# Kernel tuning notes

Measured on AMD Instinct MI355X. Metric: run time of the kernel, lower is better.

## Reference

```python
import jax, jax.numpy as jnp
import numpy as np
import math

N_EMBD = 1024
N_HEADS = 16
B, T = 4, 2048

def setup_inputs() -> dict:
    key = jax.random.key(0)
    k1, k2, k3 = jax.random.split(key, 3)
    x = jax.random.normal(k1, (B, T, N_EMBD), dtype=jnp.float32)
    scale = 1.0 / math.sqrt(N_EMBD)
    W_attn = jax.random.normal(k2, (N_EMBD, 3 * N_EMBD), dtype=jnp.float32) * scale
    W_proj = jax.random.normal(k3, (N_EMBD, N_EMBD), dtype=jnp.float32) * scale
    return {"x": x, "W_attn": W_attn, "W_proj": W_proj}

def reference(x, W_attn, W_proj):
    Bb, Tt, C = x.shape
    hd = C // N_HEADS
    qkv = x @ W_attn  # [B,T,3C]
    q, k, v = jnp.split(qkv, 3, axis=-1)
    # [B,H,T,hd]
    q = q.reshape(Bb, Tt, N_HEADS, hd).transpose(0, 2, 1, 3)
    k = k.reshape(Bb, Tt, N_HEADS, hd).transpose(0, 2, 1, 3)
    v = v.reshape(Bb, Tt, N_HEADS, hd).transpose(0, 2, 1, 3)
    att = jnp.einsum('bhqd,bhkd->bhqk', q, k) * (1.0 / math.sqrt(hd))
    mask = jnp.tril(jnp.ones((Tt, Tt), dtype=bool))
    att = jnp.where(mask[None, None], att, -jnp.inf)
    att = jax.nn.softmax(att, axis=-1)
    out = jnp.einsum('bhqk,bhkd->bhqd', att, v)
    out = out.transpose(0, 2, 1, 3).reshape(Bb, Tt, C)
    return out @ W_proj
```

## Files before the change

### kernel.cpp

```cpp
#include <hip/hip_runtime.h>
#include <cstddef>
#include <cstdint>

typedef __attribute__((ext_vector_type(8))) _Float16 half8;
typedef __attribute__((ext_vector_type(4))) _Float16 half4;
typedef __attribute__((ext_vector_type(4))) float f32x4;
typedef __attribute__((ext_vector_type(16))) float f32x16;

#define N_EMBD 1024
#define N_HEADS 16
#define BATCH 4
#define SEQ 2048
#define C3 3072
#define HD 64

__device__ inline uint32_t pk2(float x, float y) {
    auto h2 = __builtin_amdgcn_cvt_pkrtz(x, y);
    uint32_t u;
    __builtin_memcpy(&u, &h2, 4);
    return u;
}

__device__ inline void swap32(uint32_t& a, uint32_t& b) {
    asm volatile("v_permlane32_swap_b32 %0, %1" : "+v"(a), "+v"(b));
}

__global__ void cvt_f32_f16(const float* __restrict__ in, _Float16* __restrict__ out, int n) {
    int i = (blockIdx.x * 256 + threadIdx.x) * 4;
    if (i >= n) return;
    float4 v = *(const float4*)(in + i);
    half4 h;
    h[0] = (_Float16)v.x; h[1] = (_Float16)v.y; h[2] = (_Float16)v.z; h[3] = (_Float16)v.w;
    *(half4*)(out + i) = h;
}

__global__ void transpose_cvt(const float* __restrict__ in, _Float16* __restrict__ out,
                              int R, int Ncols) {
    __shared__ float tile[32][33];
    int n0 = blockIdx.x * 32, r0 = blockIdx.y * 32;
    int tx = threadIdx.x, ty = threadIdx.y;
#pragma unroll
    for (int i = 0; i < 32; i += 8)
        tile[ty + i][tx] = in[(size_t)(r0 + ty + i) * Ncols + n0 + tx];
    __syncthreads();
#pragma unroll
    for (int i = 0; i < 32; i += 8)
        out[(size_t)(n0 + ty + i) * R + r0 + tx] = (_Float16)tile[tx][ty + i];
}

__global__ void transpose_v(const _Float16* __restrict__ qkv, _Float16* __restrict__ vT) {
    __shared__ _Float16 tile[32][36];
    int t0 = blockIdx.x * 32;
    int bhd = blockIdx.y;
    int bh = bhd >> 1, dh = bhd & 1;
    int b = bh >> 4, h = bh & 15;
    int tx = threadIdx.x, ty = threadIdx.y;
#pragma unroll
    for (int i = 0; i < 32; i += 8)
        tile[ty + i][tx] = qkv[(size_t)(b * SEQ + t0 + ty + i) * C3 + 2 * N_EMBD + h * HD + dh * 32 + tx];
    __syncthreads();
#pragma unroll
    for (int i = 0; i < 32; i += 8)
        vT[((size_t)bh * HD + dh * 32 + ty + i) * SEQ + t0 + tx] = tile[tx][ty + i];
}

__device__ inline void store1(float* p, float v) { *p = v; }
__device__ inline void store1(_Float16* p, float v) { *p = (_Float16)v; }

template <typename OutT>
__global__ __launch_bounds__(512, 1) void gemm256(
    const _Float16* __restrict__ A, const _Float16* __restrict__ Bt,
    OutT* __restrict__ C, int M, int N, int K) {
    __shared__ _Float16 Al[2][256 * 64];
    __shared__ _Float16 Bl[2][256 * 64];
    const int tid = threadIdx.x;
    const int lane = tid & 63, wave = tid >> 6;
    const int l15 = lane & 15, l4 = lane >> 4;
    const int wm = wave >> 2, wn = wave & 3;

    const int nwg = gridDim.x, nbx = N >> 8;
    int wg = blockIdx.x;
    if ((nwg & 7) == 0) { int cpx = nwg >> 3; wg = (wg & 7) * cpx + (wg >> 3); }
    const int row0 = (wg / nbx) * 256, col0 = (wg % nbx) * 256;
    const int TAU = K >> 6;

    auto stageA = [&](int h, int ts) {
        _Float16* dst = &Al[ts & 1][h * 128 * 64];
#pragma unroll
        for (int i = 0; i < 2; ++i) {
            int idx = tid + 512 * i;
            int usrc = (idx & 7) ^ ((idx >> 3) & 7);
            __builtin_amdgcn_global_load_lds(
                (const __attribute__((address_space(1))) void*)(A + (size_t)(row0 + h * 128 + (idx >> 3)) * K + ts * 64 + usrc * 8),
                (__attribute__((address_space(3))) void*)(dst + idx * 8), 16, 0, 0);
        }
    };
    auto stageB = [&](int h, int ts) {
        _Float16* dst = &Bl[ts & 1][h * 128 * 64];
#pragma unroll
        for (int i = 0; i < 2; ++i) {
            int idx = tid + 512 * i;
            int usrc = (idx & 7) ^ ((idx >> 3) & 7);
            __builtin_amdgcn_global_load_lds(
                (const __attribute__((address_space(1))) void*)(Bt + (size_t)(col0 + h * 128 + (idx >> 3)) * K + ts * 64 + usrc * 8),
                (__attribute__((address_space(3))) void*)(dst + idx * 8), 16, 0, 0);
        }
    };

    f32x4 acc[8][4] = {};
    stageA(0, 0); stageA(1, 0); stageB(0, 0); stageB(1, 0);
    stageA(0, 1); stageA(1, 1); stageB(0, 1); stageB(1, 1);
    asm volatile("s_waitcnt vmcnt(8)" ::: "memory");
    __builtin_amdgcn_s_barrier();

    half8 a[4][2], b0[2][2], b1[2][2];
    for (int tau = 0; tau < TAU; ++tau) {
        const int buf = tau & 1;
        const _Float16* Ab = &Al[buf][0];
        const _Float16* Bb = &Bl[buf][0];
        const int t2ok = (tau + 2 < TAU);

#pragma unroll
        for (int m = 0; m < 4; ++m)
#pragma unroll
            for (int ks = 0; ks < 2; ++ks) {
                int r = wm * 128 + m * 16 + l15;
                a[m][ks] = *(const half8*)(Ab + r * 64 + (((ks * 4 + l4) ^ (r & 7)) * 8));
            }
#pragma unroll
        for (int n = 0; n < 2; ++n)
#pragma unroll
            for (int ks = 0; ks < 2; ++ks) {
                int r = wn * 64 + n * 16 + l15;
                b0[n][ks] = *(const half8*)(Bb + r * 64 + (((ks * 4 + l4) ^ (r & 7)) * 8));
            }
        if (tau + 1 >= 2 && tau + 1 < TAU) stageA(1, tau + 1);
        __builtin_amdgcn_s_barrier();
        __builtin_amdgcn_s_setprio(1);
#pragma unroll
        for (int m = 0; m < 4; ++m)
#pragma unroll
            for (int n = 0; n < 2; ++n)
#pragma unroll
                for (int ks = 0; ks < 2; ++ks)
                    acc[m][n] = __builtin_amdgcn_mfma_f32_16x16x32_f16(a[m][ks], b0[n][ks], acc[m][n], 0, 0, 0);
        __builtin_amdgcn_s_setprio(0);
        __builtin_amdgcn_s_barrier();

#pragma unroll
        for (int n = 0; n < 2; ++n)
#pragma unroll
            for (int ks = 0; ks < 2; ++ks) {
                int r = wn * 64 + 32 + n * 16 + l15;
                b1[n][ks] = *(const half8*)(Bb + r * 64 + (((ks * 4 + l4) ^ (r & 7)) * 8));
            }
        if (t2ok) stageB(0, tau + 2);
        __builtin_amdgcn_s_barrier();
        __builtin_amdgcn_s_setprio(1);
#pragma unroll
        for (int m = 0; m < 4; ++m)
#pragma unroll
            for (int n = 0; n < 2; ++n)
#pragma unroll
                for (int ks = 0; ks < 2; ++ks)
                    acc[m][2 + n] = __builtin_amdgcn_mfma_f32_16x16x32_f16(a[m][ks], b1[n][ks], acc[m][2 + n], 0, 0, 0);
        __builtin_amdgcn_s_setprio(0);
        __builtin_amdgcn_s_barrier();

#pragma unroll
        for (int m = 0; m < 4; ++m)
#pragma unroll
            for (int ks = 0; ks < 2; ++ks) {
                int r = wm * 128 + 64 + m * 16 + l15;
                a[m][ks] = *(const half8*)(Ab + r * 64 + (((ks * 4 + l4) ^ (r & 7)) * 8));
            }
        if (t2ok) stageB(1, tau + 2);
        __builtin_amdgcn_s_barrier();
        __builtin_amdgcn_s_setprio(1);
#pragma unroll
        for (int m = 0; m < 4; ++m)
#pragma unroll
            for (int n = 0; n < 2; ++n)
#pragma unroll
                for (int ks = 0; ks < 2; ++ks)
                    acc[4 + m][2 + n] = __builtin_amdgcn_mfma_f32_16x16x32_f16(a[m][ks], b1[n][ks], acc[4 + m][2 + n], 0, 0, 0);
        __builtin_amdgcn_s_setprio(0);
        __builtin_amdgcn_s_barrier();

        if (t2ok) stageA(0, tau + 2);
        __builtin_amdgcn_s_barrier();
        __builtin_amdgcn_s_setprio(1);
#pragma unroll
        for (int m = 0; m < 4; ++m)
#pragma unroll
            for (int n = 0; n < 2; ++n)
#pragma unroll
                for (int ks = 0; ks < 2; ++ks)
                    acc[4 + m][n] = __builtin_amdgcn_mfma_f32_16x16x32_f16(a[m][ks], b0[n][ks], acc[4 + m][n], 0, 0, 0);
        __builtin_amdgcn_s_setprio(0);
        if (tau <= TAU - 3) {
            asm volatile("s_waitcnt vmcnt(6)" ::: "memory");
        } else if (tau == TAU - 2) {
            asm volatile("s_waitcnt vmcnt(0)" ::: "memory");
        }
        __builtin_amdgcn_s_barrier();
    }

#pragma unroll
    for (int mi = 0; mi < 8; ++mi)
#pragma unroll
        for (int ni = 0; ni < 4; ++ni)
#pragma unroll
            for (int j = 0; j < 4; ++j) {
                int r = row0 + wm * 128 + (mi >> 2) * 64 + (mi & 3) * 16 + l4 * 4 + j;
                int c = col0 + wn * 64 + (ni >> 1) * 32 + (ni & 1) * 16 + l15;
                store1(C + (size_t)r * N + c, acc[mi][ni][j]);
            }
}

template <typename OutT>
__global__ __launch_bounds__(256, 2) void gemm_h(
    const _Float16* __restrict__ A, const _Float16* __restrict__ Bt,
    OutT* __restrict__ C, int M, int N, int K) {
    __shared__ _Float16 Al[128 * 32];
    __shared__ _Float16 Bl[128 * 32];
    const int tid = threadIdx.x;
    const int wave = tid >> 6, lane = tid & 63;
    const int l15 = lane & 15, l4 = lane >> 4;
    const int gx = gridDim.x;
    int lin = blockIdx.y * gx + blockIdx.x;
    int bcol, brow;
    if ((gx & 7) == 0) {
        int cpx = gx >> 3;
        int xcd = lin & 7;
        int idx = lin >> 3;
        bcol = xcd * cpx + idx % cpx;
        brow = idx / cpx;
    } else { bcol = blockIdx.x; brow = blockIdx.y; }
    const int row0 = brow * 128, col0 = bcol * 128;
    const int wm = wave >> 1, wn = wave & 1;
    f32x4 acc[4][4] = {};
    for (int k0 = 0; k0 < K; k0 += 32) {
#pragma unroll
        for (int i = 0; i < 2; ++i) {
            int c = tid + 256 * i;
            int r = c >> 2, c8 = (c & 3) * 8;
            __builtin_amdgcn_global_load_lds(
                (const __attribute__((address_space(1))) void*)(A + (size_t)(row0 + r) * K + k0 + c8),
                (__attribute__((address_space(3))) void*)(Al + (size_t)(wave * 64 + 256 * i) * 8),
                16, 0, 0);
        }
#pragma unroll
        for (int i = 0; i < 2; ++i) {
            int c = tid + 256 * i;
            int r = c >> 2, c8 = (c & 3) * 8;
            __builtin_amdgcn_global_load_lds(
                (const __attribute__((address_space(1))) void*)(Bt + (size_t)(col0 + r) * K + k0 + c8),
                (__attribute__((address_space(3))) void*)(Bl + (size_t)(wave * 64 + 256 * i) * 8),
                16, 0, 0);
        }
        __syncthreads();
        half8 a[4], b[4];
#pragma unroll
        for (int m = 0; m < 4; ++m)
            a[m] = *(const half8*)(Al + (wm * 64 + m * 16 + l15) * 32 + l4 * 8);
#pragma unroll
        for (int n = 0; n < 4; ++n)
            b[n] = *(const half8*)(Bl + (wn * 64 + n * 16 + l15) * 32 + l4 * 8);
        __builtin_amdgcn_s_setprio(1);
#pragma unroll
        for (int m = 0; m < 4; ++m)
#pragma unroll
            for (int n = 0; n < 4; ++n)
                acc[m][n] = __builtin_amdgcn_mfma_f32_16x16x32_f16(a[m], b[n], acc[m][n], 0, 0, 0);
        __builtin_amdgcn_s_setprio(0);
        __syncthreads();
    }
#pragma unroll
    for (int m = 0; m < 4; ++m)
#pragma unroll
        for (int n = 0; n < 4; ++n)
#pragma unroll
            for (int j = 0; j < 4; ++j) {
                int r = row0 + wm * 64 + m * 16 + l4 * 4 + j;
                int cc = col0 + wn * 64 + n * 16 + l15;
                store1(C + (size_t)r * N + cc, acc[m][n][j]);
            }
}

__global__ __launch_bounds__(256, 3) void attn_kernel(const _Float16* __restrict__ qkv,
                                                      const _Float16* __restrict__ vT,
                                                      _Float16* __restrict__ ao) {
    const int bid = blockIdx.x;
    const int qt = 15 - (bid >> 6);
    const int bh = bid & 63;
    const int b = bh >> 4, h = bh & 15;
    const int tid = threadIdx.x, lane = tid & 63;
    const int wave = tid >> 6;
    const int l31 = lane & 31, L = lane >> 5;

    __shared__ _Float16 Kl[3][64 * 64];
    __shared__ _Float16 Vl[3][64 * 64];

    const float qscale = 0.125f * 1.44269504089f;
    const float NEGC = -4.0f * 1.44269504089f;

    const int q0w = qt * 128 + wave * 32;
    const int q_g = q0w + l31;
    const int nt = 2 * qt + 2;

    auto stage = [&](int t, int buf) {
#pragma unroll
        for (int i = 0; i < 2; ++i) {
            int idx = tid + 256 * i;
            int key = idx >> 3, u = idx & 7;
            int d8 = (u ^ (key & 7)) * 8;
            __builtin_amdgcn_global_load_lds(
                (const __attribute__((address_space(1))) void*)(qkv + (size_t)(b * SEQ + t * 64 + key) * C3 + N_EMBD + h * HD + d8),
                (__attribute__((address_space(3))) void*)(&Kl[buf][idx * 8]), 16, 0, 0);
        }
#pragma unroll
        for (int i = 0; i < 2; ++i) {
            int idx = tid + 256 * i;
            int d = idx >> 3, u = idx & 7;
            int k8 = (u ^ (d & 7)) * 8;
            __builtin_amdgcn_global_load_lds(
                (const __attribute__((address_space(1))) void*)(vT + ((size_t)bh * HD + d) * SEQ + t * 64 + k8),
                (__attribute__((address_space(3))) void*)(&Vl[buf][idx * 8]), 16, 0, 0);
        }
    };

    stage(0, 0);
    stage(1, 1);

    half8 qb[4];
#pragma unroll
    for (int ks = 0; ks < 4; ++ks) {
        half8 v = *(const half8*)(qkv + (size_t)(b * SEQ + q_g) * C3 + h * HD + ks * 16 + L * 8);
#pragma unroll
        for (int e = 0; e < 8; ++e) v[e] = (_Float16)((float)v[e] * qscale);
        qb[ks] = v;
    }
    half8 onesf;
#pragma unroll
    for (int e = 0; e < 8; ++e) onesf[e] = (_Float16)1.0f;

    f32x16 cinit = (f32x16)(NEGC);
    f32x16 o[2];
    o[0] = (f32x16)(0.f);
    o[1] = (f32x16)(0.f);
    f32x16 lac = (f32x16)(0.f);

    asm volatile("s_waitcnt vmcnt(4)" ::: "memory");
    __builtin_amdgcn_s_barrier();

    int cur = 0;
    for (int t = 0; t < nt; ++t) {
        const int kv0 = t * 64;
        int sb = cur + 2; if (sb >= 3) sb -= 3;
        if (t + 2 < nt) stage(t + 2, sb);

        if (kv0 <= q0w + 31) {
            const _Float16* Kb = &Kl[cur][0];
            const _Float16* Vb = &Vl[cur][0];
            f32x16 s[2];
            __builtin_amdgcn_s_setprio(1);
#pragma unroll
            for (int kb = 0; kb < 2; ++kb) {
                const int key = kb * 32 + l31;
                {
                    half8 kf = *(const half8*)(Kb + key * 64 + ((L ^ (key & 7)) * 8));
                    s[kb] = __builtin_amdgcn_mfma_f32_32x32x16_f16(kf, qb[0], cinit, 0, 0, 0);
                }
#pragma unroll
                for (int ks = 1; ks < 4; ++ks) {
                    half8 kf = *(const half8*)(Kb + key * 64 + (((ks * 2 + L) ^ (key & 7)) * 8));
                    s[kb] = __builtin_amdgcn_mfma_f32_32x32x16_f16(kf, qb[ks], s[kb], 0, 0, 0);
                }
            }
            __builtin_amdgcn_s_setprio(0);
            const bool needmask = (kv0 + 63 > q0w);
#pragma unroll
            for (int kb = 0; kb < 2; ++kb) {
#pragma unroll
                for (int r = 0; r < 16; ++r) {
                    float v = exp2f(s[kb][r]);
                    if (needmask) {
                        int key_g = kv0 + kb * 32 + (r & 3) + 8 * (r >> 2) + 4 * L;
                        v = (key_g > q_g) ? 0.f : v;
                    }
                    s[kb][r] = v;
                }
            }
            half8 paf[4];
#pragma unroll
            for (int kb = 0; kb < 2; ++kb)
#pragma unroll
                for (int hf = 0; hf < 2; ++hf) {
                    const int bse = hf * 8;
                    uint32_t a0 = pk2(s[kb][bse + 0], s[kb][bse + 1]);
                    uint32_t b0 = pk2(s[kb][bse + 4], s[kb][bse + 5]);
                    swap32(a0, b0);
                    uint32_t a1 = pk2(s[kb][bse + 2], s[kb][bse + 3]);
                    uint32_t b1 = pk2(s[kb][bse + 6], s[kb][bse + 7]);
                    swap32(a1, b1);
                    uint32_t w[4] = {a0, a1, b0, b1};
                    __builtin_memcpy(&paf[kb * 2 + hf], w, 16);
                }
            __builtin_amdgcn_s_setprio(1);
#pragma unroll
            for (int ks = 0; ks < 4; ++ks) {
                lac = __builtin_amdgcn_mfma_f32_32x32x16_f16(paf[ks], onesf, lac, 0, 0, 0);
#pragma unroll
                for (int db = 0; db < 2; ++db) {
                    const int d = db * 32 + l31;
                    half8 vb = *(const half8*)(Vb + d * 64 + (((ks * 2 + L) ^ (d & 7)) * 8));
                    o[db] = __builtin_amdgcn_mfma_f32_32x32x16_f16(paf[ks], vb, o[db], 0, 0, 0);
                }
            }
            __builtin_amdgcn_s_setprio(0);
        }

        if (t + 2 < nt) {
            asm volatile("s_waitcnt vmcnt(4)" ::: "memory");
        } else if (t + 1 < nt) {
            asm volatile("s_waitcnt vmcnt(0)" ::: "memory");
        }
        __builtin_amdgcn_s_barrier();
        ++cur; if (cur == 3) cur = 0;
    }

#pragma unroll
    for (int db = 0; db < 2; ++db)
#pragma unroll
        for (int r = 0; r < 16; ++r) {
            int qg = q0w + (r & 3) + 8 * (r >> 2) + 4 * L;
            ao[(size_t)(b * SEQ + qg) * N_EMBD + h * HD + db * 32 + l31] =
                (_Float16)(o[db][r] / lac[r]);
        }
}

extern "C" void kernel_launch(void* const* d_in, const int* in_sizes, int n_in,
                              void* d_out, int out_size, void* d_ws, size_t ws_size,
                              hipStream_t stream) {
    const float* x  = (const float*)d_in[0];
    const float* Wa = (const float*)d_in[1];
    const float* Wp = (const float*)d_in[2];
    float* out = (float*)d_out;

    const int M = BATCH * SEQ;
    _Float16* xh  = (_Float16*)d_ws;
    _Float16* WaT = xh + (size_t)M * N_EMBD;
    _Float16* WpT = WaT + (size_t)C3 * N_EMBD;
    _Float16* qkv = WpT + (size_t)N_EMBD * N_EMBD;
    _Float16* ao  = qkv + (size_t)M * C3;
    _Float16* vT  = xh;

    int nx = M * N_EMBD;
    cvt_f32_f16<<<nx / 4 / 256, 256, 0, stream>>>(x, xh, nx);
    dim3 tb(32, 8);
    transpose_cvt<<<dim3(C3 / 32, N_EMBD / 32), tb, 0, stream>>>(Wa, WaT, N_EMBD, C3);
    transpose_cvt<<<dim3(N_EMBD / 32, N_EMBD / 32), tb, 0, stream>>>(Wp, WpT, N_EMBD, N_EMBD);

    gemm256<_Float16><<<dim3((M / 256) * (C3 / 256)), 512, 0, stream>>>(xh, WaT, qkv, M, C3, N_EMBD);

    transpose_v<<<dim3(SEQ / 32, BATCH * N_HEADS * 2), tb, 0, stream>>>(qkv, vT);

    attn_kernel<<<dim3(1024), 256, 0, stream>>>(qkv, vT, ao);

    gemm_h<float><<<dim3(N_EMBD / 128, M / 128), 256, 0, stream>>>(ao, WpT, out, M, N_EMBD, N_EMBD);
}
```

Baseline: 188.5 us.

## Use 256x192 QKV GEMM tiles and software-pipeline QK with softmax-PV in attention

The QKV projection GEMM now uses 256x192 tiles. That raises the workgroup count from 384 to 512, which fills the CUs more evenly, and the staging is reorganized into 64-row units. The attention kernel moves to a 4-deep K/V LDS ring and interleaves the QK^T MFMA of tile t+1 with the exp/PV work of tile t, using two score register sets to overlap the transcendental and matrix work. To make room for the extra LDS and registers, attention occupancy drops from 3 to 2 blocks per CU.

```diff
diff --git a/kernel.cpp b/kernel.cpp
--- a/kernel.cpp
+++ b/kernel.cpp
@@ -68,57 +68,49 @@
 __device__ inline void store1(_Float16* p, float v) { *p = (_Float16)v; }
 
 template <typename OutT>
-__global__ __launch_bounds__(512, 1) void gemm256(
+__global__ __launch_bounds__(512, 1) void gemm192(
     const _Float16* __restrict__ A, const _Float16* __restrict__ Bt,
     OutT* __restrict__ C, int M, int N, int K) {
     __shared__ _Float16 Al[2][256 * 64];
-    __shared__ _Float16 Bl[2][256 * 64];
+    __shared__ _Float16 Bl[2][192 * 64];
     const int tid = threadIdx.x;
     const int lane = tid & 63, wave = tid >> 6;
     const int l15 = lane & 15, l4 = lane >> 4;
     const int wm = wave >> 2, wn = wave & 3;
 
-    const int nwg = gridDim.x, nbx = N >> 8;
+    const int nwg = gridDim.x, nbx = N / 192;
     int wg = blockIdx.x;
     if ((nwg & 7) == 0) { int cpx = nwg >> 3; wg = (wg & 7) * cpx + (wg >> 3); }
-    const int row0 = (wg / nbx) * 256, col0 = (wg % nbx) * 256;
+    const int row0 = (wg / nbx) * 256, col0 = (wg % nbx) * 192;
     const int TAU = K >> 6;
 
-    auto stageA = [&](int h, int ts) {
-        _Float16* dst = &Al[ts & 1][h * 128 * 64];
-#pragma unroll
-        for (int i = 0; i < 2; ++i) {
-            int idx = tid + 512 * i;
-            int usrc = (idx & 7) ^ ((idx >> 3) & 7);
-            __builtin_amdgcn_global_load_lds(
-                (const __attribute__((address_space(1))) void*)(A + (size_t)(row0 + h * 128 + (idx >> 3)) * K + ts * 64 + usrc * 8),
-                (__attribute__((address_space(3))) void*)(dst + idx * 8), 16, 0, 0);
-        }
-    };
-    auto stageB = [&](int h, int ts) {
-        _Float16* dst = &Bl[ts & 1][h * 128 * 64];
-#pragma unroll
-        for (int i = 0; i < 2; ++i) {
-            int idx = tid + 512 * i;
-            int usrc = (idx & 7) ^ ((idx >> 3) & 7);
-            __builtin_amdgcn_global_load_lds(
-                (const __attribute__((address_space(1))) void*)(Bt + (size_t)(col0 + h * 128 + (idx >> 3)) * K + ts * 64 + usrc * 8),
-                (__attribute__((address_space(3))) void*)(dst + idx * 8), 16, 0, 0);
-        }
-    };
-
-    f32x4 acc[8][4] = {};
-    stageA(0, 0); stageA(1, 0); stageB(0, 0); stageB(1, 0);
-    stageA(0, 1); stageA(1, 1); stageB(0, 1); stageB(1, 1);
-    asm volatile("s_waitcnt vmcnt(8)" ::: "memory");
+    const int srow = tid >> 3, su = tid & 7;
+    const int usrc8 = (su ^ (srow & 7)) * 8;
+    auto stageAu = [&](int unit, int ts) {
+        __builtin_amdgcn_global_load_lds(
+            (const __attribute__((address_space(1))) void*)(A + (size_t)(row0 + unit * 64 + srow) * K + ts * 64 + usrc8),
+            (__attribute__((address_space(3))) void*)(&Al[ts & 1][unit * 64 * 64 + tid * 8]), 16, 0, 0);
+    };
+    auto stageBu = [&](int unit, int ts) {
+        __builtin_amdgcn_global_load_lds(
+            (const __attribute__((address_space(1))) void*)(Bt + (size_t)(col0 + unit * 64 + srow) * K + ts * 64 + usrc8),
+            (__attribute__((address_space(3))) void*)(&Bl[ts & 1][unit * 64 * 64 + tid * 8]), 16, 0, 0);
+    };
+    auto stageTile = [&](int ts) {
+        stageAu(0, ts); stageAu(1, ts); stageAu(2, ts); stageAu(3, ts);
+        stageBu(0, ts); stageBu(1, ts); stageBu(2, ts);
+    };
+
+    f32x4 acc[8][3] = {};
+    stageTile(0); stageTile(1);
+    asm volatile("s_waitcnt vmcnt(7)" ::: "memory");
     __builtin_amdgcn_s_barrier();
 
-    half8 a[4][2], b0[2][2], b1[2][2];
+    half8 a[4][2], b[3][2];
     for (int tau = 0; tau < TAU; ++tau) {
-        const int buf = tau & 1;
-        const _Float16* Ab = &Al[buf][0];
-        const _Float16* Bb = &Bl[buf][0];
-        const int t2ok = (tau + 2 < TAU);
+        const _Float16* Ab = &Al[tau & 1][0];
+        const _Float16* Bb = &Bl[tau & 1][0];
+        const bool t2 = (tau + 2 < TAU);
 
 #pragma unroll
         for (int m = 0; m < 4; ++m)
@@ -128,13 +120,12 @@
                 a[m][ks] = *(const half8*)(Ab + r * 64 + (((ks * 4 + l4) ^ (r & 7)) * 8));
             }
 #pragma unroll
-        for (int n = 0; n < 2; ++n)
+        for (int n = 0; n < 3; ++n)
 #pragma unroll
             for (int ks = 0; ks < 2; ++ks) {
-                int r = wn * 64 + n * 16 + l15;
-                b0[n][ks] = *(const half8*)(Bb + r * 64 + (((ks * 4 + l4) ^ (r & 7)) * 8));
-            }
-        if (tau + 1 >= 2 && tau + 1 < TAU) stageA(1, tau + 1);
+                int r = wn * 48 + n * 16 + l15;
+                b[n][ks] = *(const half8*)(Bb + r * 64 + (((ks * 4 + l4) ^ (r & 7)) * 8));
+            }
         __builtin_amdgcn_s_barrier();
         __builtin_amdgcn_s_setprio(1);
 #pragma unroll
@@ -143,27 +134,18 @@
             for (int n = 0; n < 2; ++n)
 #pragma unroll
                 for (int ks = 0; ks < 2; ++ks)
-                    acc[m][n] = __builtin_amdgcn_mfma_f32_16x16x32_f16(a[m][ks], b0[n][ks], acc[m][n], 0, 0, 0);
-        __builtin_amdgcn_s_setprio(0);
-        __builtin_amdgcn_s_barrier();
-
-#pragma unroll
-        for (int n = 0; n < 2; ++n)
-#pragma unroll
-            for (int ks = 0; ks < 2; ++ks) {
-                int r = wn * 64 + 32 + n * 16 + l15;
-                b1[n][ks] = *(const half8*)(Bb + r * 64 + (((ks * 4 + l4) ^ (r & 7)) * 8));
-            }
-        if (t2ok) stageB(0, tau + 2);
-        __builtin_amdgcn_s_barrier();
-        __builtin_amdgcn_s_setprio(1);
-#pragma unroll
-        for (int m = 0; m < 4; ++m)
-#pragma unroll
-            for (int n = 0; n < 2; ++n)
-#pragma unroll
-                for (int ks = 0; ks < 2; ++ks)
-                    acc[m][2 + n] = __builtin_amdgcn_mfma_f32_16x16x32_f16(a[m][ks], b1[n][ks], acc[m][2 + n], 0, 0, 0);
+                    acc[m][n] = __builtin_amdgcn_mfma_f32_16x16x32_f16(a[m][ks], b[n][ks], acc[m][n], 0, 0, 0);
+        __builtin_amdgcn_s_setprio(0);
+        __builtin_amdgcn_s_barrier();
+
+        if (t2) { stageBu(0, tau + 2); stageBu(1, tau + 2); stageBu(2, tau + 2); }
+        __builtin_amdgcn_s_barrier();
+        __builtin_amdgcn_s_setprio(1);
+#pragma unroll
+        for (int m = 0; m < 4; ++m)
+#pragma unroll
+            for (int ks = 0; ks < 2; ++ks)
+                acc[m][2] = __builtin_amdgcn_mfma_f32_16x16x32_f16(a[m][ks], b[2][ks], acc[m][2], 0, 0, 0);
         __builtin_amdgcn_s_setprio(0);
         __builtin_amdgcn_s_barrier();
 
@@ -174,7 +156,7 @@
                 int r = wm * 128 + 64 + m * 16 + l15;
                 a[m][ks] = *(const half8*)(Ab + r * 64 + (((ks * 4 + l4) ^ (r & 7)) * 8));
             }
-        if (t2ok) stageB(1, tau + 2);
+        if (t2) { stageAu(0, tau + 2); stageAu(2, tau + 2); }
         __builtin_amdgcn_s_barrier();
         __builtin_amdgcn_s_setprio(1);
 #pragma unroll
@@ -183,23 +165,21 @@
             for (int n = 0; n < 2; ++n)
 #pragma unroll
                 for (int ks = 0; ks < 2; ++ks)
-                    acc[4 + m][2 + n] = __builtin_amdgcn_mfma_f32_16x16x32_f16(a[m][ks], b1[n][ks], acc[4 + m][2 + n], 0, 0, 0);
-        __builtin_amdgcn_s_setprio(0);
-        __builtin_amdgcn_s_barrier();
-
-        if (t2ok) stageA(0, tau + 2);
-        __builtin_amdgcn_s_barrier();
-        __builtin_amdgcn_s_setprio(1);
-#pragma unroll
-        for (int m = 0; m < 4; ++m)
-#pragma unroll
-            for (int n = 0; n < 2; ++n)
-#pragma unroll
-                for (int ks = 0; ks < 2; ++ks)
-                    acc[4 + m][n] = __builtin_amdgcn_mfma_f32_16x16x32_f16(a[m][ks], b0[n][ks], acc[4 + m][n], 0, 0, 0);
+                    acc[4 + m][n] = __builtin_amdgcn_mfma_f32_16x16x32_f16(a[m][ks], b[n][ks], acc[4 + m][n], 0, 0, 0);
+        __builtin_amdgcn_s_setprio(0);
+        __builtin_amdgcn_s_barrier();
+
+        if (t2) { stageAu(1, tau + 2); stageAu(3, tau + 2); }
+        __builtin_amdgcn_s_barrier();
+        __builtin_amdgcn_s_setprio(1);
+#pragma unroll
+        for (int m = 0; m < 4; ++m)
+#pragma unroll
+            for (int ks = 0; ks < 2; ++ks)
+                acc[4 + m][2] = __builtin_amdgcn_mfma_f32_16x16x32_f16(a[m][ks], b[2][ks], acc[4 + m][2], 0, 0, 0);
         __builtin_amdgcn_s_setprio(0);
         if (tau <= TAU - 3) {
-            asm volatile("s_waitcnt vmcnt(6)" ::: "memory");
+            asm volatile("s_waitcnt vmcnt(7)" ::: "memory");
         } else if (tau == TAU - 2) {
             asm volatile("s_waitcnt vmcnt(0)" ::: "memory");
         }
@@ -209,11 +189,11 @@
 #pragma unroll
     for (int mi = 0; mi < 8; ++mi)
 #pragma unroll
-        for (int ni = 0; ni < 4; ++ni)
+        for (int ni = 0; ni < 3; ++ni)
 #pragma unroll
             for (int j = 0; j < 4; ++j) {
                 int r = row0 + wm * 128 + (mi >> 2) * 64 + (mi & 3) * 16 + l4 * 4 + j;
-                int c = col0 + wn * 64 + (ni >> 1) * 32 + (ni & 1) * 16 + l15;
+                int c = col0 + wn * 48 + ni * 16 + l15;
                 store1(C + (size_t)r * N + c, acc[mi][ni][j]);
             }
 }
@@ -288,7 +268,7 @@
             }
 }
 
-__global__ __launch_bounds__(256, 3) void attn_kernel(const _Float16* __restrict__ qkv,
+__global__ __launch_bounds__(256, 2) void attn_kernel(const _Float16* __restrict__ qkv,
                                                       const _Float16* __restrict__ vT,
                                                       _Float16* __restrict__ ao) {
     const int bid = blockIdx.x;
@@ -299,8 +279,8 @@
     const int wave = tid >> 6;
     const int l31 = lane & 31, L = lane >> 5;
 
-    __shared__ _Float16 Kl[3][64 * 64];
-    __shared__ _Float16 Vl[3][64 * 64];
+    __shared__ _Float16 Kl[4][64 * 64];
+    __shared__ _Float16 Vl[4][64 * 64];
 
     const float qscale = 0.125f * 1.44269504089f;
     const float NEGC = -4.0f * 1.44269504089f;
@@ -345,90 +325,106 @@
 #pragma unroll
     for (int e = 0; e < 8; ++e) onesf[e] = (_Float16)1.0f;
 
-    f32x16 cinit = (f32x16)(NEGC);
+    const f32x16 cinit = (f32x16)(NEGC);
     f32x16 o[2];
     o[0] = (f32x16)(0.f);
     o[1] = (f32x16)(0.f);
     f32x16 lac = (f32x16)(0.f);
-
-    asm volatile("s_waitcnt vmcnt(4)" ::: "memory");
+    f32x16 sE[2], sO[2];
+
+    auto qk = [&](int t, f32x16 (&s)[2]) {
+        if (t * 64 > q0w + 31) return;
+        const _Float16* Kb = &Kl[t & 3][0];
+        __builtin_amdgcn_s_setprio(1);
+#pragma unroll
+        for (int kb = 0; kb < 2; ++kb) {
+            const int key = kb * 32 + l31;
+            {
+                half8 kf = *(const half8*)(Kb + key * 64 + ((L ^ (key & 7)) * 8));
+                s[kb] = __builtin_amdgcn_mfma_f32_32x32x16_f16(kf, qb[0], cinit, 0, 0, 0);
+            }
+#pragma unroll
+            for (int ks = 1; ks < 4; ++ks) {
+                half8 kf = *(const half8*)(Kb + key * 64 + (((ks * 2 + L) ^ (key & 7)) * 8));
+                s[kb] = __builtin_amdgcn_mfma_f32_32x32x16_f16(kf, qb[ks], s[kb], 0, 0, 0);
+            }
+        }
+        __builtin_amdgcn_s_setprio(0);
+    };
+
+    auto finish = [&](int t, f32x16 (&s)[2]) {
+        if (t * 64 > q0w + 31) return;
+        const int kv0 = t * 64;
+        const _Float16* Vb = &Vl[t & 3][0];
+        const bool needmask = (kv0 + 63 > q0w);
+#pragma unroll
+        for (int kb = 0; kb < 2; ++kb) {
+#pragma unroll
+            for (int r = 0; r < 16; ++r) {
+                float v = exp2f(s[kb][r]);
+                if (needmask) {
+                    int key_g = kv0 + kb * 32 + (r & 3) + 8 * (r >> 2) + 4 * L;
+                    v = (key_g > q_g) ? 0.f : v;
+                }
+                s[kb][r] = v;
+            }
+        }
+        half8 paf[4];
+#pragma unroll
+        for (int kb = 0; kb < 2; ++kb)
+#pragma unroll
+            for (int hf = 0; hf < 2; ++hf) {
+                const int bse = hf * 8;
+                uint32_t a0 = pk2(s[kb][bse + 0], s[kb][bse + 1]);
+                uint32_t b0 = pk2(s[kb][bse + 4], s[kb][bse + 5]);
+                swap32(a0, b0);
+                uint32_t a1 = pk2(s[kb][bse + 2], s[kb][bse + 3]);
+                uint32_t b1 = pk2(s[kb][bse + 6], s[kb][bse + 7]);
+                swap32(a1, b1);
+                uint32_t w[4] = {a0, a1, b0, b1};
+                __builtin_memcpy(&paf[kb * 2 + hf], w, 16);
+            }
+        __builtin_amdgcn_s_setprio(1);
+#pragma unroll
+        for (int ks = 0; ks < 4; ++ks) {
+            lac = __builtin_amdgcn_mfma_f32_32x32x16_f16(paf[ks], onesf, lac, 0, 0, 0);
+#pragma unroll
+            for (int db = 0; db < 2; ++db) {
+                const int d = db * 32 + l31;
+                half8 vb = *(const half8*)(Vb + d * 64 + (((ks * 2 + L) ^ (d & 7)) * 8));
+                o[db] = __builtin_amdgcn_mfma_f32_32x32x16_f16(paf[ks], vb, o[db], 0, 0, 0);
+            }
+        }
+        __builtin_amdgcn_s_setprio(0);
+    };
+
+    asm volatile("s_waitcnt vmcnt(8)" ::: "memory");
     __builtin_amdgcn_s_barrier();
 
-    int cur = 0;
-    for (int t = 0; t < nt; ++t) {
-        const int kv0 = t * 64;
-        int sb = cur + 2; if (sb >= 3) sb -= 3;
-        if (t + 2 < nt) stage(t + 2, sb);
-
-        if (kv0 <= q0w + 31) {
-            const _Float16* Kb = &Kl[cur][0];
-            const _Float16* Vb = &Vl[cur][0];
-            f32x16 s[2];
-            __builtin_amdgcn_s_setprio(1);
-#pragma unroll
-            for (int kb = 0; kb < 2; ++kb) {
-                const int key = kb * 32 + l31;
-                {
-                    half8 kf = *(const half8*)(Kb + key * 64 + ((L ^ (key & 7)) * 8));
-                    s[kb] = __builtin_amdgcn_mfma_f32_32x32x16_f16(kf, qb[0], cinit, 0, 0, 0);
-                }
-#pragma unroll
-                for (int ks = 1; ks < 4; ++ks) {
-                    half8 kf = *(const half8*)(Kb + key * 64 + (((ks * 2 + L) ^ (key & 7)) * 8));
-                    s[kb] = __builtin_amdgcn_mfma_f32_32x32x16_f16(kf, qb[ks], s[kb], 0, 0, 0);
-                }
-            }
-            __builtin_amdgcn_s_setprio(0);
-            const bool needmask = (kv0 + 63 > q0w);
-#pragma unroll
-            for (int kb = 0; kb < 2; ++kb) {
-#pragma unroll
-                for (int r = 0; r < 16; ++r) {
-                    float v = exp2f(s[kb][r]);
-                    if (needmask) {
-                        int key_g = kv0 + kb * 32 + (r & 3) + 8 * (r >> 2) + 4 * L;
-                        v = (key_g > q_g) ? 0.f : v;
-                    }
-                    s[kb][r] = v;
-                }
-            }
-            half8 paf[4];
-#pragma unroll
-            for (int kb = 0; kb < 2; ++kb)
-#pragma unroll
-                for (int hf = 0; hf < 2; ++hf) {
-                    const int bse = hf * 8;
-                    uint32_t a0 = pk2(s[kb][bse + 0], s[kb][bse + 1]);
-                    uint32_t b0 = pk2(s[kb][bse + 4], s[kb][bse + 5]);
-                    swap32(a0, b0);
-                    uint32_t a1 = pk2(s[kb][bse + 2], s[kb][bse + 3]);
-                    uint32_t b1 = pk2(s[kb][bse + 6], s[kb][bse + 7]);
-                    swap32(a1, b1);
-                    uint32_t w[4] = {a0, a1, b0, b1};
-                    __builtin_memcpy(&paf[kb * 2 + hf], w, 16);
-                }
-            __builtin_amdgcn_s_setprio(1);
-#pragma unroll
-            for (int ks = 0; ks < 4; ++ks) {
-                lac = __builtin_amdgcn_mfma_f32_32x32x16_f16(paf[ks], onesf, lac, 0, 0, 0);
-#pragma unroll
-                for (int db = 0; db < 2; ++db) {
-                    const int d = db * 32 + l31;
-                    half8 vb = *(const half8*)(Vb + d * 64 + (((ks * 2 + L) ^ (d & 7)) * 8));
-                    o[db] = __builtin_amdgcn_mfma_f32_32x32x16_f16(paf[ks], vb, o[db], 0, 0, 0);
-                }
-            }
-            __builtin_amdgcn_s_setprio(0);
-        }
-
-        if (t + 2 < nt) {
-            asm volatile("s_waitcnt vmcnt(4)" ::: "memory");
-        } else if (t + 1 < nt) {
-            asm volatile("s_waitcnt vmcnt(0)" ::: "memory");
-        }
-        __builtin_amdgcn_s_barrier();
-        ++cur; if (cur == 3) cur = 0;
+    if (nt > 2) stage(2, 2);
+    qk(0, sE);
+    if (nt > 2) { asm volatile("s_waitcnt vmcnt(4)" ::: "memory"); }
+    else        { asm volatile("s_waitcnt vmcnt(0)" ::: "memory"); }
+    __builtin_amdgcn_s_barrier();
+
+    int u = 1;
+    for (; u + 1 < nt; u += 2) {
+        if (u + 2 < nt) stage(u + 2, (u + 2) & 3);
+        qk(u, sO);
+        finish(u - 1, sE);
+        if (u + 2 < nt) { asm volatile("s_waitcnt vmcnt(4)" ::: "memory"); }
+        else            { asm volatile("s_waitcnt vmcnt(0)" ::: "memory"); }
+        __builtin_amdgcn_s_barrier();
+        if (u + 3 < nt) stage(u + 3, (u + 3) & 3);
+        qk(u + 1, sE);
+        finish(u, sO);
+        if (u + 3 < nt) { asm volatile("s_waitcnt vmcnt(4)" ::: "memory"); }
+        else            { asm volatile("s_waitcnt vmcnt(0)" ::: "memory"); }
+        __builtin_amdgcn_s_barrier();
     }
+    qk(nt - 1, sO);
+    finish(nt - 2, sE);
+    finish(nt - 1, sO);
 
 #pragma unroll
     for (int db = 0; db < 2; ++db)
@@ -462,7 +458,7 @@
     transpose_cvt<<<dim3(C3 / 32, N_EMBD / 32), tb, 0, stream>>>(Wa, WaT, N_EMBD, C3);
     transpose_cvt<<<dim3(N_EMBD / 32, N_EMBD / 32), tb, 0, stream>>>(Wp, WpT, N_EMBD, N_EMBD);
 
-    gemm256<_Float16><<<dim3((M / 256) * (C3 / 256)), 512, 0, stream>>>(xh, WaT, qkv, M, C3, N_EMBD);
+    gemm192<_Float16><<<dim3((M / 256) * (C3 / 192)), 512, 0, stream>>>(xh, WaT, qkv, M, C3, N_EMBD);
 
     transpose_v<<<dim3(SEQ / 32, BATCH * N_HEADS * 2), tb, 0, stream>>>(qkv, vT);
 
```

Result: slower. 194.3 us (+3.1%).
